# Performance work log

Measured on AMD Instinct MI355X. Metric: run time of the kernel, lower is better.

Reference implementation:

```python
import jax, jax.numpy as jnp
import numpy as np

W_SEG = 2048   # segment length w
R = 4          # dilation rate
OFFSET = 0     # offset < r
H = 16         # num heads
C = 1024       # embed dim
M = W_SEG // R # tokens attended per segment


def _mha(xi, w_in, b_in, w_out, b_out):
    # xi: (b, s, m, c) -> causal multi-head self-attention per segment
    b, s, m, c = xi.shape
    dh = c // H
    qkv = jnp.einsum('bsmc,ec->bsme', xi, w_in) + b_in  # e = 3c
    q, k, v = jnp.split(qkv, 3, axis=-1)
    q = q.reshape(b, s, m, H, dh)
    k = k.reshape(b, s, m, H, dh)
    v = v.reshape(b, s, m, H, dh)
    scores = jnp.einsum('bsqhd,bskhd->bshqk', q, k) / jnp.sqrt(jnp.asarray(dh, xi.dtype))
    causal = jnp.tril(jnp.ones((m, m), dtype=bool))
    scores = jnp.where(causal, scores, jnp.asarray(-1e9, xi.dtype))
    p = jax.nn.softmax(scores, axis=-1)
    o = jnp.einsum('bshqk,bskhd->bsqhd', p, v).reshape(b, s, m, c)
    return jnp.einsum('bsmc,oc->bsmo', o, w_out) + b_out


def setup_inputs() -> dict:
    key = jax.random.key(0)
    k1, k2, k3, k4, k5 = jax.random.split(key, 5)
    x = jax.random.normal(k1, (4, 8192, C), dtype=jnp.float32)
    w_in = jax.random.normal(k2, (3 * C, C), dtype=jnp.float32) * (C ** -0.5)
    b_in = jnp.zeros((3 * C,), dtype=jnp.float32)
    w_out = jax.random.normal(k3, (C, C), dtype=jnp.float32) * (C ** -0.5)
    b_out = jnp.zeros((C,), dtype=jnp.float32)
    return {"x": x, "w_in": w_in, "b_in": b_in, "w_out": w_out, "b_out": b_out}


def reference(x, w_in, b_in, w_out, b_out):
    b, n, c = x.shape
    s = n // W_SEG  # number of segments
    xr = x.reshape(b, s, W_SEG, c)
    xi = xr[:, :, OFFSET::R, :]                # (b, s, m, c) dilated gather
    oi = _mha(xi, w_in, b_in, w_out, b_out)    # attention per segment
    out = jnp.zeros_like(xr).at[:, :, OFFSET::R, :].set(oi)  # scatter (disjoint indices)
    return out.reshape(b, n, c)
```

## Files before the change

kernel.cpp:

```cpp
#include <hip/hip_runtime.h>


typedef unsigned short u16;
typedef short short8 __attribute__((ext_vector_type(8)));
typedef short short4v __attribute__((ext_vector_type(4)));
typedef float f32x4 __attribute__((ext_vector_type(4)));

__device__ __forceinline__ u16 f2bf(float f) {
  unsigned u = __builtin_bit_cast(unsigned, f);
  u += 0x7FFFu + ((u >> 16) & 1u);
  return (u16)(u >> 16);
}

__device__ __forceinline__ void gload_lds16(const void* g, void* l) {
  __builtin_amdgcn_global_load_lds((const __attribute__((address_space(1))) void*)g,
                                   (__attribute__((address_space(3))) void*)l,
                                   16, 0, 0);
}

#define SBAR() asm volatile("s_barrier" ::: "memory")

__global__ void conv_all(const float* __restrict__ x,
                         const float* __restrict__ w_in,
                         const float* __restrict__ w_out,
                         u16* __restrict__ xi, u16* __restrict__ win,
                         u16* __restrict__ wout) {
  const int b = blockIdx.x;
  if (b < 4096) {
    int t = b * 256 + threadIdx.x;
    int row = t >> 7;
    int col = (t & 127) << 3;
    size_t src = ((size_t)((row >> 9) << 11) + ((row & 511) << 2)) * 1024 + col;
    float4 v0 = *(const float4*)(x + src);
    float4 v1 = *(const float4*)(x + src + 4);
    short8 o;
    o[0] = f2bf(v0.x); o[1] = f2bf(v0.y); o[2] = f2bf(v0.z); o[3] = f2bf(v0.w);
    o[4] = f2bf(v1.x); o[5] = f2bf(v1.y); o[6] = f2bf(v1.z); o[7] = f2bf(v1.w);
    *(short8*)(xi + (size_t)row * 1024 + col) = o;
  } else {
    const float* src;
    u16* dst;
    int t;
    if (b < 5632) { t = (b - 4096) * 256 + threadIdx.x; src = w_in;  dst = win; }
    else          { t = (b - 5632) * 256 + threadIdx.x; src = w_out; dst = wout; }
    size_t base = (size_t)t * 8;
    float4 v0 = *(const float4*)(src + base);
    float4 v1 = *(const float4*)(src + base + 4);
    short8 o;
    o[0] = f2bf(v0.x); o[1] = f2bf(v0.y); o[2] = f2bf(v0.z); o[3] = f2bf(v0.w);
    o[4] = f2bf(v1.x); o[5] = f2bf(v1.y); o[6] = f2bf(v1.z); o[7] = f2bf(v1.w);
    *(short8*)(dst + base) = o;
  }
}

template <int NCOLS, int MODE>
__global__ __launch_bounds__(512) void gemm_pipe(
    const u16* __restrict__ A, const u16* __restrict__ B,
    const float* __restrict__ bias, void* __restrict__ Cout) {
  constexpr int K = 1024, NT = 16, NTILE = NCOLS / 256;
  __shared__ u16 lds[3][24576];

  const int tid = threadIdx.x;
  const int w = tid >> 6, lane = tid & 63;
  const int wm = w >> 2, wn = w & 3;
  const int g = lane >> 4, lq = lane & 15;

  const int per = gridDim.x >> 3;
  const int s = (blockIdx.x & 7) * per + (blockIdx.x >> 3);
  const int m0 = (s / NTILE) * 128, n0 = (s % NTILE) * 256;

  const int srow = w * 8 + (lane >> 3);
  const int jch = (lane & 7) ^ ((lane >> 3) & 7);
  const u16* Ab = A + (size_t)(m0 + srow) * K + jch * 8;
  const u16* Bb = B + (size_t)(n0 + srow) * K + jch * 8;
  const int ldst = w * 512 + lane * 8;

#define SA(buf_, qd, kt) gload_lds16(Ab + (size_t)(qd) * 64 * K + (kt) * 64, &lds[buf_][(qd) * 4096 + ldst])
#define SB(buf_, qd, kt) gload_lds16(Bb + (size_t)(qd) * 64 * K + (kt) * 64, &lds[buf_][8192 + (qd) * 4096 + ldst])
#define STAGE6(kt)                                                                 \
  { const int nb_ = (kt) % 3;                                                      \
    SA(nb_, 0, kt); SA(nb_, 1, kt);                                                \
    SB(nb_, 0, kt); SB(nb_, 1, kt); SB(nb_, 2, kt); SB(nb_, 3, kt); }

  const int xw = lq & 7;
  const int arow = wm * 64 + lq;
  const int brow = wn * 64 + lq;

#define READ_TILE(aset, bset, tile_)                                               \
  { const int bufr = (tile_) % 3;                                                  \
    _Pragma("unroll") for (int kc = 0; kc < 2; ++kc) {                             \
      _Pragma("unroll") for (int mi = 0; mi < 4; ++mi)                             \
        aset[mi + 4 * kc] = *(const short8*)(                                      \
            &lds[bufr][(arow + mi * 16) * 64 + ((kc * 4 + g) ^ xw) * 8]);          \
      _Pragma("unroll") for (int ni = 0; ni < 4; ++ni)                             \
        bset[ni + 4 * kc] = *(const short8*)(                                      \
            &lds[bufr][8192 + (brow + ni * 16) * 64 + ((kc * 4 + g) ^ xw) * 8]);   \
    } }

#define MFMA_TILE(aset, bset)                                                      \
  __builtin_amdgcn_s_setprio(1);                                                   \
  _Pragma("unroll") for (int kc = 0; kc < 2; ++kc)                                 \
    _Pragma("unroll") for (int mi = 0; mi < 4; ++mi)                               \
      _Pragma("unroll") for (int ni = 0; ni < 4; ++ni)                             \
        acc[mi][ni] = __builtin_amdgcn_mfma_f32_16x16x32_bf16(                     \
            aset[mi + 4 * kc], bset[ni + 4 * kc], acc[mi][ni], 0, 0, 0);           \
  __builtin_amdgcn_s_setprio(0);

  f32x4 acc[4][4] = {};
  short8 aA[8], bA[8], aB[8], bB[8];

  STAGE6(0); STAGE6(1);
  asm volatile("s_waitcnt vmcnt(6)" ::: "memory");
  SBAR();
  READ_TILE(aA, bA, 0);

#pragma unroll 1
  for (int tt = 0; tt < NT; tt += 2) {
    if (tt + 2 < NT) STAGE6(tt + 2);
    if (tt + 2 < NT) { asm volatile("s_waitcnt vmcnt(6)" ::: "memory"); }
    else             { asm volatile("s_waitcnt vmcnt(0)" ::: "memory"); }
    asm volatile("s_waitcnt lgkmcnt(0)" ::: "memory");
    SBAR();
    READ_TILE(aB, bB, tt + 1);
    MFMA_TILE(aA, bA);

    if (tt + 3 < NT) STAGE6(tt + 3);
    if (tt + 3 < NT) { asm volatile("s_waitcnt vmcnt(6)" ::: "memory"); }
    else             { asm volatile("s_waitcnt vmcnt(0)" ::: "memory"); }
    asm volatile("s_waitcnt lgkmcnt(0)" ::: "memory");
    SBAR();
    if (tt + 2 < NT) READ_TILE(aA, bA, tt + 2);
    MFMA_TILE(aB, bB);
  }

  if (MODE == 0) {
    u16* C = (u16*)Cout;
    if (n0 < 2048) {
#pragma unroll
      for (int mi = 0; mi < 4; ++mi) {
#pragma unroll
        for (int ni = 0; ni < 4; ++ni) {
          const int col = n0 + wn * 64 + ni * 16 + lq;
          const float bv = bias[col];
          u16* dst = C + (size_t)(col >> 10) * 8388608 + (col & 1023);
#pragma unroll
          for (int r = 0; r < 4; ++r) {
            const int m = m0 + wm * 64 + mi * 16 + g * 4 + r;
            dst[(size_t)m * 1024] = f2bf(acc[mi][ni][r] + bv);
          }
        }
      }
    } else {
      u16* vt = C + 16777216;
#pragma unroll
      for (int mi = 0; mi < 4; ++mi) {
        const int m4 = m0 + wm * 64 + mi * 16 + g * 4;
        const int bs = m4 >> 9, k = m4 & 511;
#pragma unroll
        for (int ni = 0; ni < 4; ++ni) {
          const int cv = n0 - 2048 + wn * 64 + ni * 16 + lq;
          const int h = cv >> 6, d = cv & 63;
          const float bv = bias[cv + 2048];
          short4v pk;
#pragma unroll
          for (int r = 0; r < 4; ++r) pk[r] = (short)f2bf(acc[mi][ni][r] + bv);
          *(short4v*)(&vt[(size_t)((bs * 16 + h) * 64 + d) * 512 + k]) = pk;
        }
      }
    }
  } else {
    float* O = (float*)Cout;
#pragma unroll
    for (int mi = 0; mi < 4; ++mi) {
#pragma unroll
      for (int ni = 0; ni < 4; ++ni) {
        const int col = n0 + wn * 64 + ni * 16 + lq;
        const float bv = bias[col];
#pragma unroll
        for (int r = 0; r < 4; ++r) {
          const int m = m0 + wm * 64 + mi * 16 + g * 4 + r;
          const int orow = ((m >> 9) << 11) + ((m & 511) << 2);
          O[(size_t)orow * 1024 + col] = acc[mi][ni][r] + bv;
        }
      }
    }
    for (int i = 0; i < 48; ++i) {
      const int idx = i * 512 + tid;
      const int z = idx >> 13;
      const int mm = (idx & 8191) >> 6;
      const int ch = idx & 63;
      const int m = m0 + mm;
      const int orow = ((m >> 9) << 11) + ((m & 511) << 2) + 1 + z;
      *(float4*)(O + (size_t)orow * 1024 + n0 + ch * 4) =
          make_float4(0.f, 0.f, 0.f, 0.f);
    }
  }
#undef SA
#undef SB
#undef STAGE6
#undef READ_TILE
#undef MFMA_TILE
}

__global__ __launch_bounds__(512) void attn_kernel(const u16* __restrict__ qkv,
                                                   u16* __restrict__ o_ws) {
  __shared__ u16 Ks[512 * 64];
  __shared__ u16 Vs[64 * 512];
  __shared__ u16 Pl[8][16][40];

  const int tid = threadIdx.x;
  const int w = tid >> 6, lane = tid & 63;
  const int g = lane >> 4, lq = lane & 15;
  const int bh = blockIdx.x;
  const int bs = bh >> 4, h = bh & 15;

  const u16* baseq = qkv + (size_t)bs * 512 * 1024 + h * 64;
  const u16* basek = qkv + 8388608 + (size_t)bs * 512 * 1024 + h * 64;
  const u16* vhead = qkv + 16777216 + (size_t)bh * 32768;

  {
    const int rsub = lane >> 3;
    const int csw = (lane & 7) ^ rsub;
#pragma unroll
    for (int i = 0; i < 8; ++i) {
      const int step = i * 8 + w;
      gload_lds16(basek + (size_t)(step * 8 + rsub) * 1024 + csw * 8,
                  &Ks[step * 512 + lane * 8]);
    }
#pragma unroll
    for (int i = 0; i < 8; ++i) {
      const int d = i * 8 + w;
      gload_lds16(vhead + (size_t)d * 512 + (lane ^ (d & 7)) * 8,
                  &Vs[d * 512 + lane * 8]);
    }
  }
  __syncthreads();

  const int xw = lq & 7;
#pragma unroll 1
  for (int qi = 0; qi < 4; ++qi) {
    const int qt = ((qi & 1) ? (15 - w) : w) + (qi >> 1) * 16;
    const int q0 = qt * 16;
    const short8 qf0 = *(const short8*)(baseq + (size_t)(q0 + lq) * 1024 + g * 8);
    const short8 qf1 = *(const short8*)(baseq + (size_t)(q0 + lq) * 1024 + 32 + g * 8);
    f32x4 oacc[4] = {};
    float l_r[4] = {0.f, 0.f, 0.f, 0.f};
    const int nst = (qt + 2) >> 1;
#pragma unroll 1
    for (int kk = 0; kk < nst; ++kk) {
      const int kb = kk * 32;
      const bool last = (kk == nst - 1);
      f32x4 s[2];
#pragma unroll
      for (int tt = 0; tt < 2; ++tt) {
        const int r = kb + tt * 16 + lq;
        short8 klo = *(const short8*)(&Ks[r * 64 + ((g ^ xw) * 8)]);
        short8 khi = *(const short8*)(&Ks[r * 64 + (((4 + g) ^ xw) * 8)]);
        f32x4 z = {};
        z = __builtin_amdgcn_mfma_f32_16x16x32_bf16(qf0, klo, z, 0, 0, 0);
        z = __builtin_amdgcn_mfma_f32_16x16x32_bf16(qf1, khi, z, 0, 0, 0);
        s[tt] = z;
      }
#pragma unroll
      for (int tt = 0; tt < 2; ++tt) {
#pragma unroll
        for (int r = 0; r < 4; ++r) {
          float p = __expf(s[tt][r] * 0.125f);
          if (last && (kb + tt * 16 + lq > q0 + g * 4 + r)) p = 0.f;
          l_r[r] += p;
          Pl[w][g * 4 + r][tt * 16 + lq] = f2bf(p);
        }
      }
      short8 pf = *(const short8*)(&Pl[w][lq][g * 8]);
#pragma unroll
      for (int dt = 0; dt < 4; ++dt) {
        const int vr = dt * 16 + lq;
        short8 vf = *(const short8*)(&Vs[vr * 512 + ((((kb >> 3) + g) ^ xw) * 8)]);
        oacc[dt] = __builtin_amdgcn_mfma_f32_16x16x32_bf16(pf, vf, oacc[dt], 0, 0, 0);
      }
    }
#pragma unroll
    for (int r = 0; r < 4; ++r) {
      float l = l_r[r];
      l += __shfl_xor(l, 1);
      l += __shfl_xor(l, 2);
      l += __shfl_xor(l, 4);
      l += __shfl_xor(l, 8);
      const float inv = 1.0f / l;
      const int q = q0 + g * 4 + r;
      u16* dst = o_ws + (size_t)(bs * 512 + q) * 1024 + h * 64;
#pragma unroll
      for (int dt = 0; dt < 4; ++dt) dst[dt * 16 + lq] = f2bf(oacc[dt][r] * inv);
    }
  }
}

extern "C" void kernel_launch(void* const* d_in, const int* in_sizes, int n_in,
                              void* d_out, int out_size, void* d_ws, size_t ws_size,
                              hipStream_t stream) {
  const float* x     = (const float*)d_in[0];
  const float* w_in  = (const float*)d_in[1];
  const float* b_in  = (const float*)d_in[2];
  const float* w_out = (const float*)d_in[3];
  const float* b_out = (const float*)d_in[4];

  char* ws = (char*)d_ws;
  u16* xi_bf   = (u16*)(ws);
  u16* win_bf  = (u16*)(ws + 16777216);
  u16* wout_bf = (u16*)(ws + 16777216 + 6291456);
  u16* qkv     = (u16*)(ws + 16777216 + 6291456 + 2097152);
  u16* o_bf    = (u16*)(ws + 16777216 + 6291456 + 2097152 + 50331648);

  conv_all<<<6144, 256, 0, stream>>>(x, w_in, w_out, xi_bf, win_bf, wout_bf);
  gemm_pipe<3072, 0><<<768, 512, 0, stream>>>(xi_bf, win_bf, b_in, qkv);
  attn_kernel<<<256, 512, 0, stream>>>(qkv, o_bf);
  gemm_pipe<1024, 1><<<256, 512, 0, stream>>>(o_bf, wout_bf, b_out, d_out);
}
```

Measured before the change: 135.7 us.

## Use 256x256 tiles with a double-buffered interleaved pipeline for the QKV GEMM

Replaces the templated GEMM used for the QKV projection with a dedicated kernel. It uses 256x256 output tiles (each wave computes 128x64), double-buffered LDS, and global-to-LDS loads staged in sub-chunks interleaved with MFMA phases, with setprio around the MFMA blocks. The larger tile increases operand reuse and halves the block count, which cuts global and L2 traffic. In exchange it adds more accumulator registers and more barriers, and 384 blocks means fewer waves than CUs provide, so occupancy may suffer. The output-projection GEMM is split out unchanged as a non-templated kernel.

New measurement: 145.6 us. 1.07x slower.

```diff
diff --git a/kernel.cpp b/kernel.cpp
--- a/kernel.cpp
+++ b/kernel.cpp
@@ -53,21 +53,141 @@
   }
 }
 
-template <int NCOLS, int MODE>
-__global__ __launch_bounds__(512) void gemm_pipe(
+__global__ __launch_bounds__(512, 1) void gemm_qkv256(
     const u16* __restrict__ A, const u16* __restrict__ B,
-    const float* __restrict__ bias, void* __restrict__ Cout) {
-  constexpr int K = 1024, NT = 16, NTILE = NCOLS / 256;
-  __shared__ u16 lds[3][24576];
+    const float* __restrict__ bias, u16* __restrict__ C) {
+  constexpr int K = 1024, NT = 16;
+  __shared__ u16 lds[2][32768];
 
   const int tid = threadIdx.x;
   const int w = tid >> 6, lane = tid & 63;
   const int wm = w >> 2, wn = w & 3;
   const int g = lane >> 4, lq = lane & 15;
 
+  const int s = (blockIdx.x & 7) * 48 + (blockIdx.x >> 3);
+  const int m0 = (s / 12) * 256, n0 = (s % 12) * 256;
+
+  const int srow = w * 8 + (lane >> 3);
+  const int jch = (lane & 7) ^ (srow & 7);
+  const u16* Ab = A + (size_t)(m0 + srow) * K + jch * 8;
+  const u16* Bb = B + (size_t)(n0 + srow) * K + jch * 8;
+  const int ldst = w * 512 + lane * 8;
+
+#define SA(buf_, q, kt) gload_lds16(Ab + (size_t)(q) * 64 * K + (kt) * 64, &lds[buf_][(q) * 4096 + ldst])
+#define SB(buf_, q, kt) gload_lds16(Bb + (size_t)(q) * 64 * K + (kt) * 64, &lds[buf_][16384 + (q) * 4096 + ldst])
+
+  const int xw = lq & 7;
+  const int arow = wm * 128 + lq;
+  const int brow = wn * 64 + lq;
+
+#define RDA(mh, kc)                                                                \
+  _Pragma("unroll") for (int mi = 0; mi < 4; ++mi)                                 \
+    af[mi] = *(const short8*)(&lds[buf][(arow + (mh) * 64 + mi * 16) * 64 + (((kc) * 4 + g) ^ xw) * 8]);
+#define RDB(kc)                                                                    \
+  _Pragma("unroll") for (int ni = 0; ni < 4; ++ni)                                 \
+    bf[ni] = *(const short8*)(&lds[buf][16384 + (brow + ni * 16) * 64 + (((kc) * 4 + g) ^ xw) * 8]);
+#define MF16(mh)                                                                   \
+  __builtin_amdgcn_s_setprio(1);                                                   \
+  _Pragma("unroll") for (int mi = 0; mi < 4; ++mi)                                 \
+    _Pragma("unroll") for (int ni = 0; ni < 4; ++ni)                               \
+      acc[(mh) * 4 + mi][ni] = __builtin_amdgcn_mfma_f32_16x16x32_bf16(            \
+          af[mi], bf[ni], acc[(mh) * 4 + mi][ni], 0, 0, 0);                        \
+  __builtin_amdgcn_s_setprio(0);
+
+  f32x4 acc[8][4] = {};
+  short8 af[4], bf[4];
+
+  SA(0, 0, 0); SA(0, 2, 0); SB(0, 0, 0); SB(0, 1, 0); SB(0, 2, 0); SB(0, 3, 0);
+  SA(0, 1, 0); SA(0, 3, 0);
+  asm volatile("s_waitcnt vmcnt(2)" ::: "memory");
+  SBAR();
+
+#pragma unroll 1
+  for (int t = 0; t < NT; ++t) {
+    const int buf = t & 1, nb = buf ^ 1;
+    const bool more = (t + 1 < NT);
+
+    if (more) { SA(nb, 0, t + 1); SA(nb, 2, t + 1); SB(nb, 0, t + 1); }
+    RDA(0, 0); RDB(0);
+    SBAR();
+    MF16(0);
+    SBAR();
+
+    if (more) { SB(nb, 1, t + 1); SB(nb, 2, t + 1); SB(nb, 3, t + 1); }
+    RDA(1, 0);
+    if (more) { asm volatile("s_waitcnt vmcnt(3)" ::: "memory"); }
+    else      { asm volatile("s_waitcnt vmcnt(0)" ::: "memory"); }
+    SBAR();
+    MF16(1);
+    SBAR();
+
+    if (more) { SA(nb, 1, t + 1); SA(nb, 3, t + 1); }
+    RDA(0, 1); RDB(1);
+    SBAR();
+    MF16(0);
+    SBAR();
+
+    RDA(1, 1);
+    if (more) { asm volatile("s_waitcnt vmcnt(2)" ::: "memory"); }
+    SBAR();
+    MF16(1);
+    SBAR();
+  }
+
+  if (n0 < 2048) {
+#pragma unroll
+    for (int ma = 0; ma < 8; ++ma) {
+#pragma unroll
+      for (int ni = 0; ni < 4; ++ni) {
+        const int col = n0 + wn * 64 + ni * 16 + lq;
+        const float bv = bias[col];
+        u16* dst = C + (size_t)(col >> 10) * 8388608 + (col & 1023);
+#pragma unroll
+        for (int r = 0; r < 4; ++r) {
+          const int m = m0 + wm * 128 + ma * 16 + g * 4 + r;
+          dst[(size_t)m * 1024] = f2bf(acc[ma][ni][r] + bv);
+        }
+      }
+    }
+  } else {
+    u16* vt = C + 16777216;
+#pragma unroll
+    for (int ma = 0; ma < 8; ++ma) {
+      const int m4 = m0 + wm * 128 + ma * 16 + g * 4;
+      const int bs = m4 >> 9, k = m4 & 511;
+#pragma unroll
+      for (int ni = 0; ni < 4; ++ni) {
+        const int cv = n0 - 2048 + wn * 64 + ni * 16 + lq;
+        const int h = cv >> 6, d = cv & 63;
+        const float bv = bias[cv + 2048];
+        short4v pk;
+#pragma unroll
+        for (int r = 0; r < 4; ++r) pk[r] = (short)f2bf(acc[ma][ni][r] + bv);
+        *(short4v*)(&vt[(size_t)((bs * 16 + h) * 64 + d) * 512 + k]) = pk;
+      }
+    }
+  }
+#undef SA
+#undef SB
+#undef RDA
+#undef RDB
+#undef MF16
+}
+
+__global__ __launch_bounds__(512) void gemm_out(
+    const u16* __restrict__ A, const u16* __restrict__ B,
+    const float* __restrict__ bias, float* __restrict__ O) {
+  constexpr int K = 1024, NT = 16;
+  __shared__ u16 lds[3][24576];
+
+  const int tid = threadIdx.x;
+  const int w = tid >> 6, lane = tid & 63;
+  const int wm = w >> 2, wn = w & 3;
+  const int g = lane >> 4, lq = lane & 15;
+
   const int per = gridDim.x >> 3;
   const int s = (blockIdx.x & 7) * per + (blockIdx.x >> 3);
-  const int m0 = (s / NTILE) * 128, n0 = (s % NTILE) * 256;
+  const int m0 = (s >> 2) * 128, n0 = (s & 3) * 256;
 
   const int srow = w * 8 + (lane >> 3);
   const int jch = (lane & 7) ^ ((lane >> 3) & 7);
@@ -133,67 +253,29 @@
     MFMA_TILE(aB, bB);
   }
 
-  if (MODE == 0) {
-    u16* C = (u16*)Cout;
-    if (n0 < 2048) {
-#pragma unroll
-      for (int mi = 0; mi < 4; ++mi) {
-#pragma unroll
-        for (int ni = 0; ni < 4; ++ni) {
-          const int col = n0 + wn * 64 + ni * 16 + lq;
-          const float bv = bias[col];
-          u16* dst = C + (size_t)(col >> 10) * 8388608 + (col & 1023);
-#pragma unroll
-          for (int r = 0; r < 4; ++r) {
-            const int m = m0 + wm * 64 + mi * 16 + g * 4 + r;
-            dst[(size_t)m * 1024] = f2bf(acc[mi][ni][r] + bv);
-          }
-        }
-      }
-    } else {
-      u16* vt = C + 16777216;
-#pragma unroll
-      for (int mi = 0; mi < 4; ++mi) {
-        const int m4 = m0 + wm * 64 + mi * 16 + g * 4;
-        const int bs = m4 >> 9, k = m4 & 511;
-#pragma unroll
-        for (int ni = 0; ni < 4; ++ni) {
-          const int cv = n0 - 2048 + wn * 64 + ni * 16 + lq;
-          const int h = cv >> 6, d = cv & 63;
-          const float bv = bias[cv + 2048];
-          short4v pk;
-#pragma unroll
-          for (int r = 0; r < 4; ++r) pk[r] = (short)f2bf(acc[mi][ni][r] + bv);
-          *(short4v*)(&vt[(size_t)((bs * 16 + h) * 64 + d) * 512 + k]) = pk;
-        }
-      }
-    }
-  } else {
-    float* O = (float*)Cout;
-#pragma unroll
-    for (int mi = 0; mi < 4; ++mi) {
-#pragma unroll
-      for (int ni = 0; ni < 4; ++ni) {
-        const int col = n0 + wn * 64 + ni * 16 + lq;
-        const float bv = bias[col];
-#pragma unroll
-        for (int r = 0; r < 4; ++r) {
-          const int m = m0 + wm * 64 + mi * 16 + g * 4 + r;
-          const int orow = ((m >> 9) << 11) + ((m & 511) << 2);
-          O[(size_t)orow * 1024 + col] = acc[mi][ni][r] + bv;
-        }
-      }
-    }
-    for (int i = 0; i < 48; ++i) {
-      const int idx = i * 512 + tid;
-      const int z = idx >> 13;
-      const int mm = (idx & 8191) >> 6;
-      const int ch = idx & 63;
-      const int m = m0 + mm;
-      const int orow = ((m >> 9) << 11) + ((m & 511) << 2) + 1 + z;
-      *(float4*)(O + (size_t)orow * 1024 + n0 + ch * 4) =
-          make_float4(0.f, 0.f, 0.f, 0.f);
-    }
+#pragma unroll
+  for (int mi = 0; mi < 4; ++mi) {
+#pragma unroll
+    for (int ni = 0; ni < 4; ++ni) {
+      const int col = n0 + wn * 64 + ni * 16 + lq;
+      const float bv = bias[col];
+#pragma unroll
+      for (int r = 0; r < 4; ++r) {
+        const int m = m0 + wm * 64 + mi * 16 + g * 4 + r;
+        const int orow = ((m >> 9) << 11) + ((m & 511) << 2);
+        O[(size_t)orow * 1024 + col] = acc[mi][ni][r] + bv;
+      }
+    }
+  }
+  for (int i = 0; i < 48; ++i) {
+    const int idx = i * 512 + tid;
+    const int z = idx >> 13;
+    const int mm = (idx & 8191) >> 6;
+    const int ch = idx & 63;
+    const int m = m0 + mm;
+    const int orow = ((m >> 9) << 11) + ((m & 511) << 2) + 1 + z;
+    *(float4*)(O + (size_t)orow * 1024 + n0 + ch * 4) =
+        make_float4(0.f, 0.f, 0.f, 0.f);
   }
 #undef SA
 #undef SB
@@ -312,7 +394,7 @@
   u16* o_bf    = (u16*)(ws + 16777216 + 6291456 + 2097152 + 50331648);
 
   conv_all<<<6144, 256, 0, stream>>>(x, w_in, w_out, xi_bf, win_bf, wout_bf);
-  gemm_pipe<3072, 0><<<768, 512, 0, stream>>>(xi_bf, win_bf, b_in, qkv);
+  gemm_qkv256<<<384, 512, 0, stream>>>(xi_bf, win_bf, b_in, qkv);
   attn_kernel<<<256, 512, 0, stream>>>(qkv, o_bf);
-  gemm_pipe<1024, 1><<<256, 512, 0, stream>>>(o_bf, wout_bf, b_out, d_out);
-}
+  gemm_out<<<256, 512, 0, stream>>>(o_bf, wout_bf, b_out, (float*)d_out);
+}
```
